# Kernel tuning notes

Measured on AMD Instinct MI355X. Metric: run time of the kernel, lower is better.

## Reference

```python
import jax, jax.numpy as jnp
import numpy as np

B, T, H = 128, 256, 512


def setup_inputs() -> dict:
    key = jax.random.key(0)
    ks = jax.random.split(key, 9)
    s = 0.05  # small init scale to keep tanh/softmax well-conditioned
    return {
        "enc_output": jax.random.normal(ks[0], (B, T, H), jnp.float32),
        "h0": jax.random.normal(ks[1], (B, H), jnp.float32) * s,
        "c0": jax.random.normal(ks[2], (B, H), jnp.float32) * s,
        "W1": jax.random.normal(ks[3], (H, H), jnp.float32) * s,
        "W2": jax.random.normal(ks[4], (H, H), jnp.float32) * s,
        "V": jax.random.normal(ks[5], (H,), jnp.float32) * s,
        "Wk": jax.random.normal(ks[6], (T, 4 * H), jnp.float32) * s,  # LSTM input kernel (input = last_pointer, dim T)
        "Wr": jax.random.normal(ks[7], (H, 4 * H), jnp.float32) * s,  # LSTM recurrent kernel
        "b": jnp.zeros((4 * H,), jnp.float32),
    }


def reference(enc_output, h0, c0, W1, W2, V, Wk, Wr, b):
    Bq, Tq, Hq = enc_output.shape
    # Precompute W1 @ encoder outputs (constant across decode steps; same math)
    w1_e = jnp.einsum("bth,hd->btd", enc_output, W1)  # [B,T,H]

    def step(carry, _):
        h, c, lp = carry  # h,c: [B,H]; lp (last pointer probs): [B,T]
        z = lp @ Wk + h @ Wr + b  # [B,4H], keras gate order i,f,g,o
        i, f, g, o = jnp.split(z, 4, axis=-1)
        c_new = jax.nn.sigmoid(f) * c + jax.nn.sigmoid(i) * jnp.tanh(g)
        h_new = jax.nn.sigmoid(o) * jnp.tanh(c_new)
        # Bahdanau additive attention -> pointer distribution over T
        w2_d = h_new @ W2  # [B,H]
        score = jnp.einsum("bth,h->bt", jnp.tanh(w1_e + w2_d[:, None, :]), V)  # [B,T]
        probs = jax.nn.softmax(score, axis=1)
        return (h_new, c_new, probs), probs

    lp0 = jnp.ones((Bq, Tq), enc_output.dtype)
    _, outs = jax.lax.scan(step, (h0, c0, lp0), None, length=Tq)  # [T,B,T]
    return jnp.transpose(outs, (1, 0, 2))  # [B, T(steps), T(pointers)]
```

## Files before the change

### kernel.cpp

```cpp
#include <hip/hip_runtime.h>
#include <hip/hip_bf16.h>
#include <cstddef>

#define B_ 128
#define T_ 256
#define H_ 512
#define H4_ 2048

__device__ __forceinline__ float rcp_f(float x) { return __builtin_amdgcn_rcpf(x); }
__device__ __forceinline__ float sigf(float x) { return rcp_f(1.0f + __expf(-x)); }
__device__ __forceinline__ float tanh_f(float x) {
  float p = __expf(x + x);
  return fmaf(-2.0f, rcp_f(1.0f + p), 1.0f);
}
__device__ __forceinline__ float4 ld4(const float* p) { return *reinterpret_cast<const float4*>(p); }
__device__ __forceinline__ void st4(float* p, float4 v) { *reinterpret_cast<float4*>(p) = v; }
__device__ __forceinline__ void fma4(float4& a, float s, float4 w) {
  a.x = fmaf(s, w.x, a.x); a.y = fmaf(s, w.y, a.y);
  a.z = fmaf(s, w.z, a.z); a.w = fmaf(s, w.w, a.w);
}

__device__ __forceinline__ float ald1(const float* p) {
  return __hip_atomic_load(p, __ATOMIC_RELAXED, __HIP_MEMORY_SCOPE_AGENT);
}
__device__ __forceinline__ void ast1(float* p, float v) {
  __hip_atomic_store(p, v, __ATOMIC_RELAXED, __HIP_MEMORY_SCOPE_AGENT);
}
__device__ __forceinline__ float2 ald2(const float* p) {
  unsigned long long v = __hip_atomic_load((const unsigned long long*)p,
                                           __ATOMIC_RELAXED, __HIP_MEMORY_SCOPE_AGENT);
  union { unsigned long long u; float2 f; } c; c.u = v; return c.f;
}

union H4 { ushort4 u; _Float16 h[4]; };
union H8 { int4 v; _Float16 h[8]; };
__device__ __forceinline__ void sth4(_Float16* p, float4 v) {
  H4 c;
  c.h[0] = (_Float16)v.x; c.h[1] = (_Float16)v.y;
  c.h[2] = (_Float16)v.z; c.h[3] = (_Float16)v.w;
  *reinterpret_cast<ushort4*>(p) = c.u;
}

#define W1EH_OFF  0ull
#define WPACK_OFF 8388608ull
#define W2H_OFF   9961472ull
#define HP_OFF    10092544ull
#define HROW_OFF  10223616ull
#define EP_OFF    10289152ull
#define W2D_OFF   10321920ull
#define D2_OFF    10387456ull
#define CNT_OFF   10387968ull

__global__ __launch_bounds__(256) void w1e_kernel(const float* __restrict__ A,
                                                  const float* __restrict__ Bw,
                                                  _Float16* __restrict__ C) {
  __shared__ float As[32][68];
  __shared__ float Bs[32][68];
  const int i0 = blockIdx.x * 64;
  const int j0 = blockIdx.y * 64;
  const int tx = threadIdx.x & 15, ty = threadIdx.x >> 4;
  float4 acc0 = make_float4(0,0,0,0), acc1 = acc0, acc2 = acc0, acc3 = acc0;
  for (int k0 = 0; k0 < H_; k0 += 32) {
#pragma unroll
    for (int q = 0; q < 2; q++) {
      int idx = q * 256 + threadIdx.x;
      int ai = idx >> 3, ak = (idx & 7) << 2;
      float4 av = ld4(A + (size_t)(i0 + ai) * H_ + k0 + ak);
      As[ak][ai] = av.x; As[ak + 1][ai] = av.y; As[ak + 2][ai] = av.z; As[ak + 3][ai] = av.w;
      int bk = idx >> 4, bj = (idx & 15) << 2;
      st4(&Bs[bk][bj], ld4(Bw + (size_t)(k0 + bk) * H_ + j0 + bj));
    }
    __syncthreads();
#pragma unroll
    for (int kk = 0; kk < 32; kk++) {
      float4 a = ld4(&As[kk][ty << 2]);
      float4 bv = ld4(&Bs[kk][tx << 2]);
      fma4(acc0, a.x, bv); fma4(acc1, a.y, bv); fma4(acc2, a.z, bv); fma4(acc3, a.w, bv);
    }
    __syncthreads();
  }
  size_t base = (size_t)(i0 + (ty << 2)) * H_ + j0 + (tx << 2);
  sth4(&C[base], acc0); sth4(&C[base + H_], acc1);
  sth4(&C[base + 2 * H_], acc2); sth4(&C[base + 3 * H_], acc3);
}

__global__ __launch_bounds__(256) void pack_kernel(const float* __restrict__ Wk,
                                                   const float* __restrict__ Wr,
                                                   const float* __restrict__ W2,
                                                   float* __restrict__ Wpack,
                                                   _Float16* __restrict__ W2h,
                                                   unsigned* __restrict__ cnt) {
  const int g = blockIdx.x, tid = threadIdx.x;
#pragma unroll
  for (int it = 0; it < 24; ++it) {
    int idx = it * 256 + tid;
    int k = idx >> 3, c = idx & 7;
    int col = (c >> 1) * 512 + 2 * g + (c & 1);
    float v = (k < 256) ? Wk[(size_t)k * H4_ + col] : Wr[(size_t)(k - 256) * H4_ + col];
    Wpack[((size_t)g * 768 + k) * 8 + c] = v;
  }
#pragma unroll
  for (int it = 0; it < 4; ++it) {
    int idx = it * 65536 + g * 256 + tid;
    W2h[idx] = (_Float16)W2[idx];
  }
  if (g == 0) {
#pragma unroll
    for (int i = 0; i < 4; ++i) cnt[i * 256 + tid] = 0u;
  }
}

__device__ __forceinline__ void gridbar(unsigned* cnt, unsigned& phase, int tid, int wg) {
  asm volatile("s_waitcnt vmcnt(0)" ::: "memory");
  __syncthreads();
  if (tid == 0) {
    unsigned r1 = __hip_atomic_fetch_add(&cnt[(wg & 31) * 16], 1u,
                                         __ATOMIC_RELAXED, __HIP_MEMORY_SCOPE_AGENT);
    if (r1 == phase * 8u + 7u) {
      unsigned r2 = __hip_atomic_fetch_add(&cnt[512], 1u,
                                           __ATOMIC_RELAXED, __HIP_MEMORY_SCOPE_AGENT);
      if (r2 == phase * 32u + 31u) {
#pragma unroll
        for (int i = 0; i < 8; ++i)
          __hip_atomic_store(&cnt[768 + i * 16], phase + 1u,
                             __ATOMIC_RELAXED, __HIP_MEMORY_SCOPE_AGENT);
      }
    }
    const unsigned* rel = &cnt[768 + (wg >> 5) * 16];
    while (__hip_atomic_load(rel, __ATOMIC_RELAXED, __HIP_MEMORY_SCOPE_AGENT) <= phase)
      __builtin_amdgcn_s_sleep(2);
  }
  __syncthreads();
  ++phase;
}

__global__ __launch_bounds__(1024, 4) void decoder_persistent(
    const _Float16* __restrict__ w1eh, const float* __restrict__ Wpack,
    const _Float16* __restrict__ W2h, const float* __restrict__ Vv,
    const float* __restrict__ bias, const float* __restrict__ h0,
    const float* __restrict__ c0,
    float* __restrict__ htr,
    float* __restrict__ hrow,
    float* __restrict__ etr,
    float* __restrict__ w2dA,
    float* __restrict__ d2,
    unsigned* __restrict__ cnt,
    float* __restrict__ out) {
  __shared__ float smem[21504];
  float* zred     = smem;
  float* zfin     = smem + 12288;
  float* c_lds    = smem + 13312;
  float* bias_lds = smem + 13568;
  float* dred     = smem + 13576;

  const int g = blockIdx.x;
  const int tid = threadIdx.x;
  const int bl = tid & 127;
  const int ksu = __builtin_amdgcn_readfirstlane(tid >> 7);
  const int wv = tid >> 6, ln = tid & 63;
  const int sb = g >> 1;
  const int t0 = (g & 1) << 7;
  unsigned phase = 0;
  float epv[8];

  if (tid < 256) {
    int b = tid >> 1, jj = tid & 1;
    c_lds[b * 2 + jj] = c0[(size_t)b * H_ + 2 * g + jj];
    ast1(htr + 65536 + ((size_t)g * 128 + b) * 2 + jj, h0[(size_t)b * H_ + 2 * g + jj]);
    if (g == 0) ast1(d2 + 256 + tid, 0.5f);
  }
  if (tid < 8) bias_lds[tid] = bias[(tid >> 1) * 512 + 2 * g + (tid & 1)];
  if (g < 128) ast1(etr + g * 256 + tid, 1.0f);
  gridbar(cnt, phase, tid, g);

  const float4 v0 = ld4(Vv + (ln << 3));
  const float4 v1 = ld4(Vv + (ln << 3) + 4);

  for (int s = 0; s < 256; ++s) {
    const float* hin = htr + ((s + 1) & 1) * 65536;
    float* hout = htr + (s & 1) * 65536;
    const float* dPrev = d2 + ((s + 1) & 1) * 256;
    float* dCur = d2 + (s & 1) * 256;

    {
      float2 dd = ald2(dPrev + bl * 2);
      float rd = rcp_f(dd.x + dd.y);
      float4 accA = make_float4(0,0,0,0), accB = accA;
      float2 e0[8], e1[8];
#pragma unroll
      for (int j = 0; j < 8; ++j) {
        int k2 = ksu * 2 + j * 16;
        e0[j] = ald2(etr + k2 * 256 + bl * 2);
        e1[j] = ald2(etr + k2 * 256 + 256 + bl * 2);
      }
#pragma unroll
      for (int j = 0; j < 8; ++j) {
        int kb = ksu * 4 + j * 32;
        const float* wp = Wpack + (((size_t)g * 768 + kb) << 3);
        float4 wa0 = ld4(wp),      wb0 = ld4(wp + 4);
        float4 wa1 = ld4(wp + 8),  wb1 = ld4(wp + 12);
        float4 wa2 = ld4(wp + 16), wb2 = ld4(wp + 20);
        float4 wa3 = ld4(wp + 24), wb3 = ld4(wp + 28);
        fma4(accA, e0[j].x, wa0); fma4(accB, e0[j].x, wb0);
        fma4(accA, e0[j].y, wa1); fma4(accB, e0[j].y, wb1);
        fma4(accA, e1[j].x, wa2); fma4(accB, e1[j].x, wb2);
        fma4(accA, e1[j].y, wa3); fma4(accB, e1[j].y, wb3);
      }
      accA.x *= rd; accA.y *= rd; accA.z *= rd; accA.w *= rd;
      accB.x *= rd; accB.y *= rd; accB.z *= rd; accB.w *= rd;
#pragma unroll
      for (int half = 0; half < 2; ++half) {
        float2 p0[8], p1[8];
#pragma unroll
        for (int j = 0; j < 8; ++j) {
          int k2 = ksu * 2 + (half * 8 + j) * 16;
          p0[j] = ald2(hin + k2 * 256 + bl * 2);
          p1[j] = ald2(hin + k2 * 256 + 256 + bl * 2);
        }
#pragma unroll
        for (int j = 0; j < 8; ++j) {
          int kb = ksu * 4 + (half * 8 + j) * 32;
          const float* wp = Wpack + (((size_t)g * 768 + 256 + kb) << 3);
          float4 wa0 = ld4(wp),      wb0 = ld4(wp + 4);
          float4 wa1 = ld4(wp + 8),  wb1 = ld4(wp + 12);
          float4 wa2 = ld4(wp + 16), wb2 = ld4(wp + 20);
          float4 wa3 = ld4(wp + 24), wb3 = ld4(wp + 28);
          fma4(accA, p0[j].x, wa0); fma4(accB, p0[j].x, wb0);
          fma4(accA, p0[j].y, wa1); fma4(accB, p0[j].y, wb1);
          fma4(accA, p1[j].x, wa2); fma4(accB, p1[j].x, wb2);
          fma4(accA, p1[j].y, wa3); fma4(accB, p1[j].y, wb3);
        }
      }
      float* zr = &zred[(ksu * 128 + bl) * 12];
      st4(zr, accA); st4(zr + 4, accB);
    }
    __syncthreads();
    {
      int b = tid >> 3, cc = tid & 7;
      float zsum = bias_lds[cc];
#pragma unroll
      for (int k2 = 0; k2 < 8; ++k2) zsum += zred[(k2 * 128 + b) * 12 + cc];
      zfin[b * 8 + cc] = zsum;
    }
    __syncthreads();
    if (tid < 256) {
      int b = tid >> 1, jj = tid & 1;
      float zi = zfin[b * 8 + 0 + jj], zf = zfin[b * 8 + 2 + jj];
      float zg = zfin[b * 8 + 4 + jj], zo = zfin[b * 8 + 6 + jj];
      float cv = c_lds[b * 2 + jj];
      float cn = sigf(zf) * cv + sigf(zi) * tanh_f(zg);
      float hn = sigf(zo) * tanh_f(cn);
      c_lds[b * 2 + jj] = cn;
      ast1(hout + ((size_t)g * 128 + b) * 2 + jj, hn);
      ast1(hrow + (size_t)b * 512 + 2 * g + jj, hn);
    }
    gridbar(cnt, phase, tid, g);

    {
      const int colb = ((g & 1) << 8) + (ln << 2);
      const float* hb = hrow + (size_t)sb * 512 + (wv << 5);
      float hreg[32];
#pragma unroll
      for (int kk = 0; kk < 32; ++kk) hreg[kk] = ald1(hb + kk);
      float4 acc = make_float4(0,0,0,0);
#pragma unroll 8
      for (int kk = 0; kk < 32; ++kk) {
        H4 w; w.u = *reinterpret_cast<const ushort4*>(W2h + (size_t)((wv << 5) + kk) * 512 + colb);
        float4 wf = make_float4((float)w.h[0], (float)w.h[1], (float)w.h[2], (float)w.h[3]);
        fma4(acc, hreg[kk], wf);
      }
      st4(&zred[(wv << 8) + (ln << 2)], acc);
    }
    __syncthreads();
    if (tid < 256) {
      float sum = 0.0f;
#pragma unroll
      for (int w = 0; w < 16; ++w) sum += zred[(w << 8) + tid];
      ast1(w2dA + (size_t)sb * 512 + ((g & 1) << 8) + tid, sum);
    }
    gridbar(cnt, phase, tid, g);

    {
      const float* wrow = w2dA + (size_t)sb * 512 + (ln << 3);
      float2 a0 = ald2(wrow), a1 = ald2(wrow + 2), a2 = ald2(wrow + 4), a3 = ald2(wrow + 6);
      float4 u0 = make_float4(a0.x, a0.y, a1.x, a1.y);
      float4 u1 = make_float4(a2.x, a2.y, a3.x, a3.y);
      float2 ddp = ald2(dPrev + sb * 2);
      float rdp = rcp_f(ddp.x + ddp.y);
      const _Float16* rowb = w1eh + (((size_t)sb * 256 + t0 + (wv << 3)) << 9) + (ln << 3);
      H8 raws[8];
#pragma unroll
      for (int r = 0; r < 8; ++r)
        raws[r].v = *reinterpret_cast<const int4*>(rowb + (size_t)r * 512);
      float sc[8];
#pragma unroll
      for (int r = 0; r < 8; ++r) {
        float a;
        a = tanh_f((float)raws[r].h[0] + u0.x) * v0.x;
        a = fmaf(tanh_f((float)raws[r].h[1] + u0.y), v0.y, a);
        a = fmaf(tanh_f((float)raws[r].h[2] + u0.z), v0.z, a);
        a = fmaf(tanh_f((float)raws[r].h[3] + u0.w), v0.w, a);
        a = fmaf(tanh_f((float)raws[r].h[4] + u1.x), v1.x, a);
        a = fmaf(tanh_f((float)raws[r].h[5] + u1.y), v1.y, a);
        a = fmaf(tanh_f((float)raws[r].h[6] + u1.z), v1.z, a);
        a = fmaf(tanh_f((float)raws[r].h[7] + u1.w), v1.w, a);
#pragma unroll
        for (int m = 32; m > 0; m >>= 1) a += __shfl_xor(a, m, 64);
        sc[r] = a;
      }
      if (ln == 0) {
        float dacc = 0.0f;
#pragma unroll
        for (int r = 0; r < 8; ++r) {
          int t = t0 + (wv << 3) + r;
          if (s > 0) out[(size_t)sb * 65536 + (size_t)(s - 1) * 256 + t] = epv[r] * rdp;
          float ev = __expf(sc[r]);
          epv[r] = ev;
          ast1(etr + (((t >> 1) << 7) + sb) * 2 + (t & 1), ev);
          dacc += ev;
        }
        dred[wv] = dacc;
      }
    }
    __syncthreads();
    if (tid == 0) {
      float sd = 0.0f;
#pragma unroll
      for (int k = 0; k < 16; ++k) sd += dred[k];
      ast1(dCur + sb * 2 + (g & 1), sd);
    }
    gridbar(cnt, phase, tid, g);
  }

  {
    float2 ddf = ald2(d2 + 256 + sb * 2);
    float rdf = rcp_f(ddf.x + ddf.y);
    if (ln == 0) {
#pragma unroll
      for (int r = 0; r < 8; ++r) {
        int t = t0 + (wv << 3) + r;
        out[(size_t)sb * 65536 + 255ull * 256 + t] = epv[r] * rdf;
      }
    }
  }
}

extern "C" void kernel_launch(void* const* d_in, const int* in_sizes, int n_in,
                              void* d_out, int out_size, void* d_ws, size_t ws_size,
                              hipStream_t stream) {
  const float* enc  = (const float*)d_in[0];
  const float* h0   = (const float*)d_in[1];
  const float* c0   = (const float*)d_in[2];
  const float* W1   = (const float*)d_in[3];
  const float* W2   = (const float*)d_in[4];
  const float* V    = (const float*)d_in[5];
  const float* Wk   = (const float*)d_in[6];
  const float* Wr   = (const float*)d_in[7];
  const float* bias = (const float*)d_in[8];
  float* out = (float*)d_out;
  float* ws = (float*)d_ws;

  _Float16* w1eh = (_Float16*)(ws + W1EH_OFF);
  float* Wpack   = ws + WPACK_OFF;
  _Float16* W2h  = (_Float16*)(ws + W2H_OFF);
  float* htr     = ws + HP_OFF;
  float* hrow    = ws + HROW_OFF;
  float* etr     = ws + EP_OFF;
  float* w2dA    = ws + W2D_OFF;
  float* d2      = ws + D2_OFF;
  unsigned* cnt  = (unsigned*)(ws + CNT_OFF);

  pack_kernel<<<256, 256, 0, stream>>>(Wk, Wr, W2, Wpack, W2h, cnt);
  w1e_kernel<<<dim3(512, 8), 256, 0, stream>>>(enc, W1, w1eh);
  decoder_persistent<<<256, 1024, 0, stream>>>(w1eh, Wpack, W2h, V, bias, h0, c0,
                                               htr, hrow, etr, w2dA, d2, cnt, out);
}
```

Baseline: 10.08 ms.

## Compute full W2·h per workgroup locally to drop a grid barrier

```diff
diff --git a/kernel.cpp b/kernel.cpp
--- a/kernel.cpp
+++ b/kernel.cpp
@@ -47,9 +47,8 @@
 #define HP_OFF    10092544ull
 #define HROW_OFF  10223616ull
 #define EP_OFF    10289152ull
-#define W2D_OFF   10321920ull
-#define D2_OFF    10387456ull
-#define CNT_OFF   10387968ull
+#define D2_OFF    10321920ull
+#define CNT_OFF   10322432ull
 
 __global__ __launch_bounds__(256) void w1e_kernel(const float* __restrict__ A,
                                                   const float* __restrict__ Bw,
@@ -142,7 +141,6 @@
     float* __restrict__ htr,
     float* __restrict__ hrow,
     float* __restrict__ etr,
-    float* __restrict__ w2dA,
     float* __restrict__ d2,
     unsigned* __restrict__ cnt,
     float* __restrict__ out) {
@@ -152,6 +150,8 @@
   float* c_lds    = smem + 13312;
   float* bias_lds = smem + 13568;
   float* dred     = smem + 13576;
+  float* hrow_lds = smem + 13592;
+  float* w2d_lds  = smem + 14104;
 
   const int g = blockIdx.x;
   const int tid = threadIdx.x;
@@ -170,17 +170,23 @@
     if (g == 0) ast1(d2 + 256 + tid, 0.5f);
   }
   if (tid < 8) bias_lds[tid] = bias[(tid >> 1) * 512 + 2 * g + (tid & 1)];
-  if (g < 128) ast1(etr + g * 256 + tid, 1.0f);
+  if (g < 128 && tid < 256) ast1(etr + g * 256 + tid, 1.0f);
   gridbar(cnt, phase, tid, g);
 
   const float4 v0 = ld4(Vv + (ln << 3));
   const float4 v1 = ld4(Vv + (ln << 3) + 4);
+  const _Float16* rowb = w1eh + (((size_t)sb * 256 + t0 + (wv << 3)) << 9) + (ln << 3);
 
   for (int s = 0; s < 256; ++s) {
     const float* hin = htr + ((s + 1) & 1) * 65536;
     float* hout = htr + (s & 1) * 65536;
     const float* dPrev = d2 + ((s + 1) & 1) * 256;
     float* dCur = d2 + (s & 1) * 256;
+
+    H8 raws[8];
+#pragma unroll
+    for (int r = 0; r < 8; ++r)
+      raws[r].v = *reinterpret_cast<const int4*>(rowb + ((size_t)r << 9));
 
     {
       float2 dd = ald2(dPrev + bl * 2);
@@ -256,42 +262,45 @@
     }
     gridbar(cnt, phase, tid, g);
 
+    if (tid < 256) {
+      float2 hv = ald2(hrow + (size_t)sb * 512 + (tid << 1));
+      hrow_lds[(tid << 1)] = hv.x; hrow_lds[(tid << 1) + 1] = hv.y;
+    }
+    __syncthreads();
     {
-      const int colb = ((g & 1) << 8) + (ln << 2);
-      const float* hb = hrow + (size_t)sb * 512 + (wv << 5);
-      float hreg[32];
-#pragma unroll
-      for (int kk = 0; kk < 32; ++kk) hreg[kk] = ald1(hb + kk);
-      float4 acc = make_float4(0,0,0,0);
-#pragma unroll 8
-      for (int kk = 0; kk < 32; ++kk) {
-        H4 w; w.u = *reinterpret_cast<const ushort4*>(W2h + (size_t)((wv << 5) + kk) * 512 + colb);
-        float4 wf = make_float4((float)w.h[0], (float)w.h[1], (float)w.h[2], (float)w.h[3]);
-        fma4(acc, hreg[kk], wf);
-      }
-      st4(&zred[(wv << 8) + (ln << 2)], acc);
-    }
-    __syncthreads();
-    if (tid < 256) {
-      float sum = 0.0f;
-#pragma unroll
-      for (int w = 0; w < 16; ++w) sum += zred[(w << 8) + tid];
-      ast1(w2dA + (size_t)sb * 512 + ((g & 1) << 8) + tid, sum);
-    }
-    gridbar(cnt, phase, tid, g);
-
+      const int c8 = ln << 3;
+      const _Float16* wp = W2h + ((size_t)(wv << 5) << 9) + c8;
+      const float* hb = hrow_lds + (wv << 5);
+      float4 accL = make_float4(0,0,0,0), accH = accL;
+#pragma unroll 4
+      for (int k = 0; k < 32; ++k) {
+        float hk = hb[k];
+        H8 w; w.v = *reinterpret_cast<const int4*>(wp + ((size_t)k << 9));
+        accL.x = fmaf(hk, (float)w.h[0], accL.x);
+        accL.y = fmaf(hk, (float)w.h[1], accL.y);
+        accL.z = fmaf(hk, (float)w.h[2], accL.z);
+        accL.w = fmaf(hk, (float)w.h[3], accL.w);
+        accH.x = fmaf(hk, (float)w.h[4], accH.x);
+        accH.y = fmaf(hk, (float)w.h[5], accH.y);
+        accH.z = fmaf(hk, (float)w.h[6], accH.z);
+        accH.w = fmaf(hk, (float)w.h[7], accH.w);
+      }
+      st4(&zred[(wv << 9) + c8], accL);
+      st4(&zred[(wv << 9) + c8 + 4], accH);
+    }
+    __syncthreads();
+    if (tid < 512) {
+      float s16 = 0.0f;
+#pragma unroll
+      for (int q = 0; q < 16; ++q) s16 += zred[(q << 9) + tid];
+      w2d_lds[tid] = s16;
+    }
+    __syncthreads();
     {
-      const float* wrow = w2dA + (size_t)sb * 512 + (ln << 3);
-      float2 a0 = ald2(wrow), a1 = ald2(wrow + 2), a2 = ald2(wrow + 4), a3 = ald2(wrow + 6);
-      float4 u0 = make_float4(a0.x, a0.y, a1.x, a1.y);
-      float4 u1 = make_float4(a2.x, a2.y, a3.x, a3.y);
+      float4 u0 = ld4(w2d_lds + (ln << 3));
+      float4 u1 = ld4(w2d_lds + (ln << 3) + 4);
       float2 ddp = ald2(dPrev + sb * 2);
       float rdp = rcp_f(ddp.x + ddp.y);
-      const _Float16* rowb = w1eh + (((size_t)sb * 256 + t0 + (wv << 3)) << 9) + (ln << 3);
-      H8 raws[8];
-#pragma unroll
-      for (int r = 0; r < 8; ++r)
-        raws[r].v = *reinterpret_cast<const int4*>(rowb + (size_t)r * 512);
       float sc[8];
 #pragma unroll
       for (int r = 0; r < 8; ++r) {
@@ -366,12 +375,11 @@
   float* htr     = ws + HP_OFF;
   float* hrow    = ws + HROW_OFF;
   float* etr     = ws + EP_OFF;
-  float* w2dA    = ws + W2D_OFF;
   float* d2      = ws + D2_OFF;
   unsigned* cnt  = (unsigned*)(ws + CNT_OFF);
 
   pack_kernel<<<256, 256, 0, stream>>>(Wk, Wr, W2, Wpack, W2h, cnt);
   w1e_kernel<<<dim3(512, 8), 256, 0, stream>>>(enc, W1, w1eh);
   decoder_persistent<<<256, 1024, 0, stream>>>(w1eh, Wpack, W2h, V, bias, h0, c0,
-                                               htr, hrow, etr, w2dA, d2, cnt, out);
-}
+                                               htr, hrow, etr, d2, cnt, out);
+}
```

After: 10.32 ms. 1.02x slower.
